# Kernel tuning notes

Measured on AMD Instinct MI355X. Metric: run time of the kernel, lower is better.

The kernel has to match this reference:

```python
import jax, jax.numpy as jnp
import numpy as np

IN_CH = 256
QK_CH = IN_CH // 8  # 32

def setup_inputs() -> dict:
    key = jax.random.key(0)
    ks = jax.random.split(key, 7)
    x = jax.random.normal(ks[0], (4, IN_CH, 64, 64), dtype=jnp.float32)
    s_in = 1.0 / np.sqrt(IN_CH)
    # 1x1 conv weights stored as [out_ch, in_ch]; biases [out_ch]
    Wq = jax.random.uniform(ks[1], (QK_CH, IN_CH), jnp.float32, -s_in, s_in)
    bq = jax.random.uniform(ks[2], (QK_CH,), jnp.float32, -s_in, s_in)
    Wk = jax.random.uniform(ks[3], (QK_CH, IN_CH), jnp.float32, -s_in, s_in)
    bk = jax.random.uniform(ks[4], (QK_CH,), jnp.float32, -s_in, s_in)
    Wv = jax.random.uniform(ks[5], (IN_CH, IN_CH), jnp.float32, -s_in, s_in)
    bv = jax.random.uniform(ks[6], (IN_CH,), jnp.float32, -s_in, s_in)
    return {"x": x, "Wq": Wq, "bq": bq, "Wk": Wk, "bk": bk, "Wv": Wv, "bv": bv}

def reference(x, Wq, bq, Wk, bk, Wv, bv):
    n, c, h, w = x.shape
    xf = x.reshape(n, c, h * w)  # [n, c, hw]
    # 1x1 convs == per-position channel matmuls
    q = jnp.einsum('oc,ncs->nos', Wq, xf) + bq[None, :, None]  # [n, c/8, hw]
    k = jnp.einsum('oc,ncs->nos', Wk, xf) + bk[None, :, None]  # [n, c/8, hw]
    v = jnp.einsum('oc,ncs->nos', Wv, xf) + bv[None, :, None]  # [n, c,  hw]
    # energy[n, i, j] = <q[:, i], k[:, j]>  (no scaling, as in original)
    energy = jnp.einsum('nci,ncj->nij', q, k)  # [n, hw, hw]
    attention = jax.nn.softmax(energy, axis=-1)
    # out[n, c, i] = sum_j v[n, c, j] * attention[n, i, j]
    out = jnp.einsum('ncj,nij->nci', v, attention)
    return out.reshape(n, c, h, w)
```

## Files before the change

### kernel.cpp

```cpp
#include <hip/hip_runtime.h>
#include <hip/hip_bf16.h>
#include <stdint.h>
#include <stddef.h>

typedef unsigned short u16;
typedef unsigned int   u32;
typedef __attribute__((ext_vector_type(8))) short bf16x8;
typedef __attribute__((ext_vector_type(4))) float f32x4;

#define LOG2E   1.44269504f
#define EXP_OFF 23.0831206f

static __device__ __forceinline__ float bf2f(u16 v) {
    u32 u = ((u32)v) << 16; float f; __builtin_memcpy(&f, &u, 4); return f;
}
static __device__ __forceinline__ u16 f2bf(float f) {
    u32 u; __builtin_memcpy(&u, &f, 4);
    u32 r = (u + 0x7fffu + ((u >> 16) & 1u)) >> 16; return (u16)r;
}
static __device__ __forceinline__ float as_f(u32 u) { float f; __builtin_memcpy(&f, &u, 4); return f; }
static __device__ __forceinline__ u32   as_u(float f) { u32 u; __builtin_memcpy(&u, &f, 4); return u; }

static __device__ __forceinline__ int detect_f32_wave0(const void* x, int t) {
    const u32* xw = (const u32*)x;
    int bad = 0;
    #pragma unroll
    for (int k = 0; k < 4; ++k) {
        u32 wv = xw[(t << 2) + k];
        int e = (wv >> 7) & 0xff;
        bad += (e >= 160);
    }
    unsigned long long m = __ballot(bad > 0);
    return (__popcll(m) >= 8) ? 1 : 0;
}


__global__ __launch_bounds__(256) void qkv_proj_mfma(
    const void* __restrict__ x,
    const void* __restrict__ Wq, const void* __restrict__ bq,
    const void* __restrict__ Wk, const void* __restrict__ bk,
    const void* __restrict__ Wv, const void* __restrict__ bv,
    u16* __restrict__ qws, u16* __restrict__ kws, u16* __restrict__ vws,
    int n_off, int nshiftp)
{
    __shared__ u16 Wl[64 * 256];
    __shared__ int dtf;

    const int t    = threadIdx.x;
    const int bid  = blockIdx.x;
    const int n_w  = bid & ((1 << nshiftp) - 1);
    const int rest = bid >> nshiftp;
    const int g    = rest % 5;
    const int it   = rest / 5;
    const int n_g  = n_off + n_w;
    const int i0   = it << 6;

    if (t < 64) { int f = detect_f32_wave0(x, t); if (t == 0) dtf = f; }
    __syncthreads();
    const bool isf32 = (dtf != 0);

    #pragma unroll
    for (int k = 0; k < 16; ++k) {
        int idx  = t + (k << 8);
        int row  = idx >> 6;
        int col4 = (idx & 63) << 2;
        const void* src; int srow;
        if (g == 0) {
            if (row < 32) { src = Wq; srow = row; }
            else          { src = Wk; srow = row - 32; }
        } else { src = Wv; srow = ((g - 1) << 6) + row; }
        ushort4 h;
        if (isf32) {
            float4 wv = *((const float4*)((const float*)src + srow * 256 + col4));
            h.x = f2bf(wv.x); h.y = f2bf(wv.y); h.z = f2bf(wv.z); h.w = f2bf(wv.w);
        } else {
            h = *((const ushort4*)((const u16*)src + srow * 256 + col4));
        }
        *(ushort4*)&Wl[(row << 8) + (col4 ^ ((row & 7) << 3))] = h;
    }
    __syncthreads();

    const int lane = t & 63;
    const int w    = t >> 6;
    const int n16  = lane & 15;
    const int quad = lane >> 4;
    const int i_b  = i0 + (w << 4);
    const int i    = i_b + n16;
    const int swz  = (n16 & 7) << 3;

    f32x4 acc[4];
    #pragma unroll
    for (int f = 0; f < 4; ++f) acc[f] = (f32x4){0.f, 0.f, 0.f, 0.f};

    if (isf32) {
        const float* xp = (const float*)x
            + (((size_t)(n_g * 256 + (quad << 3))) << 12) + i;
        float af[8];
        #pragma unroll
        for (int e = 0; e < 8; ++e) af[e] = xp[(size_t)e << 12];
        #pragma unroll
        for (int c8 = 0; c8 < 8; ++c8) {
            bf16x8 a;
            #pragma unroll
            for (int e = 0; e < 8; ++e) a[e] = (short)f2bf(af[e]);
            if (c8 < 7) {
                const float* xn = xp + (((size_t)(c8 + 1) << 5) << 12);
                #pragma unroll
                for (int e = 0; e < 8; ++e) af[e] = xn[(size_t)e << 12];
            }
            const int c0 = c8 << 5;
            #pragma unroll
            for (int f = 0; f < 4; ++f) {
                const int brow = (f << 4) + n16;
                bf16x8 b = *(const bf16x8*)
                    &Wl[(brow << 8) + ((c0 + (quad << 3)) ^ swz)];
                acc[f] = __builtin_amdgcn_mfma_f32_16x16x32_bf16(a, b, acc[f], 0, 0, 0);
            }
        }
    } else {
        const u16* xp = (const u16*)x
            + (((size_t)(n_g * 256 + (quad << 3))) << 12) + i;
        u16 af[8];
        #pragma unroll
        for (int e = 0; e < 8; ++e) af[e] = xp[(size_t)e << 12];
        #pragma unroll
        for (int c8 = 0; c8 < 8; ++c8) {
            bf16x8 a;
            #pragma unroll
            for (int e = 0; e < 8; ++e) a[e] = (short)af[e];
            if (c8 < 7) {
                const u16* xn = xp + (((size_t)(c8 + 1) << 5) << 12);
                #pragma unroll
                for (int e = 0; e < 8; ++e) af[e] = xn[(size_t)e << 12];
            }
            const int c0 = c8 << 5;
            #pragma unroll
            for (int f = 0; f < 4; ++f) {
                const int brow = (f << 4) + n16;
                bf16x8 b = *(const bf16x8*)
                    &Wl[(brow << 8) + ((c0 + (quad << 3)) ^ swz)];
                acc[f] = __builtin_amdgcn_mfma_f32_16x16x32_bf16(a, b, acc[f], 0, 0, 0);
            }
        }
    }

    if (g == 0) {
        #pragma unroll
        for (int f = 0; f < 4; ++f) {
            const int ol   = (f << 4) + n16;
            const bool isq = (ol < 32);
            const int och  = isq ? ol : (ol - 32);
            float bias;
            if (isf32) bias = ((const float*)(isq ? bq : bk))[och];
            else       bias = bf2f(((const u16*)(isq ? bq : bk))[och]);
            u16* dst = (isq ? qws : kws) + (((size_t)n_w) << 17) + och;
            const float scale = isq ? LOG2E : 1.0f;
            #pragma unroll
            for (int r = 0; r < 4; ++r) {
                const int ii = i_b + (quad << 2) + r;
                dst[(size_t)ii << 5] = f2bf((acc[f][r] + bias) * scale);
            }
        }
    } else {
        #pragma unroll
        for (int f = 0; f < 4; ++f) {
            const int c = ((g - 1) << 6) + (f << 4) + n16;
            float bias = isf32 ? ((const float*)bv)[c]
                               : bf2f(((const u16*)bv)[c]);
            const int i4 = i_b + (quad << 2);
            ushort4 h;
            h.x = f2bf(acc[f][0] + bias);
            h.y = f2bf(acc[f][1] + bias);
            h.z = f2bf(acc[f][2] + bias);
            h.w = f2bf(acc[f][3] + bias);
            const size_t addr = ((size_t)n_w << 20)
                + ((size_t)(c >> 4) << 16)
                + ((size_t)(i4 >> 5) << 9)
                + (size_t)((((((i4 & 31) >> 3) << 4) + (c & 15)) << 3) + (i4 & 7));
            *(ushort4*)(vws + addr) = h;
        }
    }
}

__global__ __launch_bounds__(1024) void flash_mfma6(
    const u16* __restrict__ qws, const u16* __restrict__ kws,
    const u16* __restrict__ vws, void* __restrict__ out,
    const void* __restrict__ x, int n_off, int nshift)
{
    __shared__ __align__(16) char arena[17920];
    __shared__ __align__(16) float lS[64];
    __shared__ int dtf;
    u16*   PsA  = (u16*)arena;
    float* Dbuf = (float*)arena;

    const int t    = threadIdx.x;
    const int lane = t & 63;
    const int w    = t >> 6;
    const int n16  = lane & 15;
    const int quad = lane >> 4;
    const int bid  = blockIdx.x;
    const int n_w  = bid & ((1 << nshift) - 1);
    const int qt   = bid >> nshift;
    const int n_g  = n_off + n_w;
    const int i0   = qt << 6;

    if (t < 64) {
        int f = detect_f32_wave0(x, t);
        if (t == 0) dtf = f;
        lS[t] = 0.f;
    }

    const u16* qb = qws + (((size_t)n_w) << 17);
    const u16* kb = kws + (((size_t)n_w) << 17);
    const u16* vb = vws + (((size_t)n_w) << 20);

    const int qsub_s = w & 3;
    const int jsub   = w >> 2;
    const int cq = w & 7;
    const int jq = w >> 3;

    const bf16x8 qfrag =
        *(const bf16x8*)(qb + ((size_t)(i0 + (qsub_s << 4) + n16) << 5) + (quad << 3));

    f32x4 acc[4][2];
    #pragma unroll
    for (int a = 0; a < 4; ++a)
        #pragma unroll
        for (int b = 0; b < 2; ++b) acc[a][b] = (f32x4){0.f, 0.f, 0.f, 0.f};
    float lp[4] = {0.f, 0.f, 0.f, 0.f};

    const int jcol = (jsub << 4) + n16;
    const int j8   = jcol >> 3;
    const int jlo  = jcol & 7;
    const int ksw  = (jq << 2) + quad;

    const u16* vfp0 = vb + ((size_t)(cq << 1) << 16) + ((size_t)jq << 9)
                         + ((size_t)((quad << 4) + n16) << 3);
    const u16* vfp1 = vfp0 + 65536;

    bf16x8 kreg, vf0, vf1;

    kreg = *(const bf16x8*)(kb + ((size_t)((jsub << 4) + n16) << 5) + (quad << 3));
    {
        u16* Ps = PsA;
        const f32x4 z = {0.f, 0.f, 0.f, 0.f};
        f32x4 s = __builtin_amdgcn_mfma_f32_16x16x32_bf16(qfrag, kreg, z, 0, 0, 0);
        #pragma unroll
        for (int r = 0; r < 4; ++r) {
            const int qrow = (qsub_s << 4) + (quad << 2) + r;
            float p = exp2f(s[r] - EXP_OFF);
            u32 u = as_u(p) & 0xffff0000u;
            lp[r] += as_f(u);
            Ps[qrow * 64 + ((j8 ^ (qrow & 7)) << 3) + jlo] = (u16)(u >> 16);
        }
        kreg = *(const bf16x8*)(kb + ((size_t)(64 + (jsub << 4) + n16) << 5) + (quad << 3));
        vf0 = *(const bf16x8*)(vfp0);
        vf1 = *(const bf16x8*)(vfp1);
    }
    __syncthreads();

    for (int tile = 1; tile < 64; ++tile) {
        const int par  = tile & 1;
        u16* Psc = PsA + (par << 12);
        u16* Psp = PsA + ((par ^ 1) << 12);

        bf16x8 pa[4];
        #pragma unroll
        for (int qs = 0; qs < 4; ++qs) {
            const int qrow = (qs << 4) + n16;
            pa[qs] = *(const bf16x8*)&Psp[qrow * 64 + ((ksw ^ (qrow & 7)) << 3)];
        }
        #pragma unroll
        for (int qs = 0; qs < 4; ++qs) {
            acc[qs][0] = __builtin_amdgcn_mfma_f32_16x16x32_bf16(pa[qs], vf0, acc[qs][0], 0, 0, 0);
            acc[qs][1] = __builtin_amdgcn_mfma_f32_16x16x32_bf16(pa[qs], vf1, acc[qs][1], 0, 0, 0);
        }

        vf0 = *(const bf16x8*)(vfp0 + ((size_t)tile << 10));
        vf1 = *(const bf16x8*)(vfp1 + ((size_t)tile << 10));

        const f32x4 z = {0.f, 0.f, 0.f, 0.f};
        f32x4 s = __builtin_amdgcn_mfma_f32_16x16x32_bf16(qfrag, kreg, z, 0, 0, 0);
        #pragma unroll
        for (int r = 0; r < 4; ++r) {
            const int qrow = (qsub_s << 4) + (quad << 2) + r;
            float p = exp2f(s[r] - EXP_OFF);
            u32 u = as_u(p) & 0xffff0000u;
            lp[r] += as_f(u);
            Psc[qrow * 64 + ((j8 ^ (qrow & 7)) << 3) + jlo] = (u16)(u >> 16);
        }

        if (tile < 63) {
            const int j0n = (tile + 1) << 6;
            kreg = *(const bf16x8*)(kb + ((size_t)(j0n + (jsub << 4) + n16) << 5)
                                    + (quad << 3));
        }
        __syncthreads();
    }

    {
        u16* Psp = PsA + (1 << 12);
        bf16x8 pa[4];
        #pragma unroll
        for (int qs = 0; qs < 4; ++qs) {
            const int qrow = (qs << 4) + n16;
            pa[qs] = *(const bf16x8*)&Psp[qrow * 64 + ((ksw ^ (qrow & 7)) << 3)];
        }
        #pragma unroll
        for (int qs = 0; qs < 4; ++qs) {
            acc[qs][0] = __builtin_amdgcn_mfma_f32_16x16x32_bf16(pa[qs], vf0, acc[qs][0], 0, 0, 0);
            acc[qs][1] = __builtin_amdgcn_mfma_f32_16x16x32_bf16(pa[qs], vf1, acc[qs][1], 0, 0, 0);
        }
    }

    #pragma unroll
    for (int r = 0; r < 4; ++r) {
        lp[r] += __shfl_xor(lp[r], 1);
        lp[r] += __shfl_xor(lp[r], 2);
        lp[r] += __shfl_xor(lp[r], 4);
        lp[r] += __shfl_xor(lp[r], 8);
    }
    if (n16 == 0) {
        #pragma unroll
        for (int r = 0; r < 4; ++r)
            atomicAdd(&lS[(qsub_s << 4) + (quad << 2) + r], lp[r]);
    }
    __syncthreads();
    if (t < 64) lS[t] = 1.0f / lS[t];
    const bool isf32 = (dtf != 0);

    for (int chunk = 0; chunk < 4; ++chunk) {
        __syncthreads();
        if (jq == 1 && (cq >> 1) == chunk) {
            #pragma unroll
            for (int qs = 0; qs < 4; ++qs)
                #pragma unroll
                for (int cs = 0; cs < 2; ++cs)
                    *(f32x4*)&Dbuf[(((cq & 1) << 5) + (cs << 4) + n16) * 68 +
                                   (qs << 4) + (quad << 2)] = acc[qs][cs];
        }
        __syncthreads();
        if (jq == 0 && (cq >> 1) == chunk) {
            #pragma unroll
            for (int qs = 0; qs < 4; ++qs)
                #pragma unroll
                for (int cs = 0; cs < 2; ++cs) {
                    float* p = &Dbuf[(((cq & 1) << 5) + (cs << 4) + n16) * 68 +
                                     (qs << 4) + (quad << 2)];
                    f32x4 d = *(f32x4*)p;
                    d += acc[qs][cs];
                    *(f32x4*)p = d;
                }
        }
        __syncthreads();
        const int c_l = t >> 4;
        const int qg  = (t & 15) << 2;
        float4 d  = *(float4*)&Dbuf[c_l * 68 + qg];
        float4 rl = *(float4*)&lS[qg];
        const int c_glob = (chunk << 6) + c_l;
        const size_t ob = (((size_t)(n_g * 256 + c_glob)) << 12) + i0 + qg;
        if (isf32) {
            float4 o = make_float4(d.x * rl.x, d.y * rl.y, d.z * rl.z, d.w * rl.w);
            *(float4*)((float*)out + ob) = o;
        } else {
            union { uint2 v; u16 h[4]; } o;
            o.h[0] = f2bf(d.x * rl.x);
            o.h[1] = f2bf(d.y * rl.y);
            o.h[2] = f2bf(d.z * rl.z);
            o.h[3] = f2bf(d.w * rl.w);
            *(uint2*)((u16*)out + ob) = o.v;
        }
    }
}

extern "C" void kernel_launch(void* const* d_in, const int* in_sizes, int n_in,
                              void* d_out, int out_size, void* d_ws, size_t ws_size,
                              hipStream_t stream)
{
    const void* x  = d_in[0];
    const void* Wq = d_in[1];
    const void* bq = d_in[2];
    const void* Wk = d_in[3];
    const void* bk = d_in[4];
    const void* Wv = d_in[5];
    const void* bv = d_in[6];

    const size_t full_need = (size_t)(4u * 4096u) * (32 + 32 + 256) * 2;
    if (ws_size >= full_need) {
        u16* qws = (u16*)d_ws;
        u16* kws = qws + (size_t)4 * 4096 * 32;
        u16* vws = kws + (size_t)4 * 4096 * 32;
        qkv_proj_mfma<<<dim3(1280), dim3(256), 0, stream>>>(
            x, Wq, bq, Wk, bk, Wv, bv, qws, kws, vws, 0, 2);
        flash_mfma6<<<dim3(256), dim3(1024), 0, stream>>>(
            qws, kws, vws, d_out, x, 0, 2);
    } else {
        u16* qws = (u16*)d_ws;
        u16* kws = qws + (size_t)4096 * 32;
        u16* vws = kws + (size_t)4096 * 32;
        for (int n = 0; n < 4; ++n) {
            qkv_proj_mfma<<<dim3(320), dim3(256), 0, stream>>>(
                x, Wq, bq, Wk, bk, Wv, bv, qws, kws, vws, n, 0);
            flash_mfma6<<<dim3(64), dim3(1024), 0, stream>>>(
                qws, kws, vws, d_out, x, n, 0);
        }
    }
}
```

Baseline: 144.5 us.

## Halve query tile to 32 rows and drop cross-wave LDS reduction of PV

```diff
diff --git a/kernel.cpp b/kernel.cpp
--- a/kernel.cpp
+++ b/kernel.cpp
@@ -182,16 +182,14 @@
     }
 }
 
-__global__ __launch_bounds__(1024) void flash_mfma6(
+__global__ __launch_bounds__(512) void flash_mfma7(
     const u16* __restrict__ qws, const u16* __restrict__ kws,
     const u16* __restrict__ vws, void* __restrict__ out,
     const void* __restrict__ x, int n_off, int nshift)
 {
-    __shared__ __align__(16) char arena[17920];
-    __shared__ __align__(16) float lS[64];
+    __shared__ __align__(16) u16 PsA[2 * 32 * 64];
+    __shared__ __align__(16) float lS[32];
     __shared__ int dtf;
-    u16*   PsA  = (u16*)arena;
-    float* Dbuf = (float*)arena;
 
     const int t    = threadIdx.x;
     const int lane = t & 63;
@@ -202,29 +200,28 @@
     const int n_w  = bid & ((1 << nshift) - 1);
     const int qt   = bid >> nshift;
     const int n_g  = n_off + n_w;
-    const int i0   = qt << 6;
+    const int i0   = qt << 5;
 
     if (t < 64) {
         int f = detect_f32_wave0(x, t);
         if (t == 0) dtf = f;
-        lS[t] = 0.f;
-    }
+    }
+    if (t < 32) lS[t] = 0.f;
 
     const u16* qb = qws + (((size_t)n_w) << 17);
     const u16* kb = kws + (((size_t)n_w) << 17);
     const u16* vb = vws + (((size_t)n_w) << 20);
 
-    const int qsub_s = w & 3;
-    const int jsub   = w >> 2;
-    const int cq = w & 7;
-    const int jq = w >> 3;
+    const int qsub_s = w & 1;
+    const int jsub   = w >> 1;
+    const int cq = w;
 
     const bf16x8 qfrag =
         *(const bf16x8*)(qb + ((size_t)(i0 + (qsub_s << 4) + n16) << 5) + (quad << 3));
 
-    f32x4 acc[4][2];
-    #pragma unroll
-    for (int a = 0; a < 4; ++a)
+    f32x4 acc[2][2];
+    #pragma unroll
+    for (int a = 0; a < 2; ++a)
         #pragma unroll
         for (int b = 0; b < 2; ++b) acc[a][b] = (f32x4){0.f, 0.f, 0.f, 0.f};
     float lp[4] = {0.f, 0.f, 0.f, 0.f};
@@ -232,59 +229,74 @@
     const int jcol = (jsub << 4) + n16;
     const int j8   = jcol >> 3;
     const int jlo  = jcol & 7;
-    const int ksw  = (jq << 2) + quad;
-
-    const u16* vfp0 = vb + ((size_t)(cq << 1) << 16) + ((size_t)jq << 9)
-                         + ((size_t)((quad << 4) + n16) << 3);
-    const u16* vfp1 = vfp0 + 65536;
-
-    bf16x8 kreg, vf0, vf1;
+
+    const u16* vfp[2][2];
+    #pragma unroll
+    for (int cs = 0; cs < 2; ++cs)
+        #pragma unroll
+        for (int jh = 0; jh < 2; ++jh)
+            vfp[cs][jh] = vb + ((size_t)((cq << 1) + cs) << 16)
+                             + ((size_t)jh << 9)
+                             + ((size_t)((quad << 4) + n16) << 3);
+
+    bf16x8 kreg, vf[2][2];
+    const f32x4 zoff = {-EXP_OFF, -EXP_OFF, -EXP_OFF, -EXP_OFF};
 
     kreg = *(const bf16x8*)(kb + ((size_t)((jsub << 4) + n16) << 5) + (quad << 3));
     {
         u16* Ps = PsA;
-        const f32x4 z = {0.f, 0.f, 0.f, 0.f};
-        f32x4 s = __builtin_amdgcn_mfma_f32_16x16x32_bf16(qfrag, kreg, z, 0, 0, 0);
+        f32x4 s = __builtin_amdgcn_mfma_f32_16x16x32_bf16(qfrag, kreg, zoff, 0, 0, 0);
         #pragma unroll
         for (int r = 0; r < 4; ++r) {
             const int qrow = (qsub_s << 4) + (quad << 2) + r;
-            float p = exp2f(s[r] - EXP_OFF);
+            float p = exp2f(s[r]);
             u32 u = as_u(p) & 0xffff0000u;
             lp[r] += as_f(u);
             Ps[qrow * 64 + ((j8 ^ (qrow & 7)) << 3) + jlo] = (u16)(u >> 16);
         }
         kreg = *(const bf16x8*)(kb + ((size_t)(64 + (jsub << 4) + n16) << 5) + (quad << 3));
-        vf0 = *(const bf16x8*)(vfp0);
-        vf1 = *(const bf16x8*)(vfp1);
+        #pragma unroll
+        for (int cs = 0; cs < 2; ++cs)
+            #pragma unroll
+            for (int jh = 0; jh < 2; ++jh)
+                vf[cs][jh] = *(const bf16x8*)(vfp[cs][jh]);
     }
     __syncthreads();
 
     for (int tile = 1; tile < 64; ++tile) {
         const int par  = tile & 1;
-        u16* Psc = PsA + (par << 12);
-        u16* Psp = PsA + ((par ^ 1) << 12);
-
-        bf16x8 pa[4];
-        #pragma unroll
-        for (int qs = 0; qs < 4; ++qs) {
+        u16* Psc = PsA + (par << 11);
+        u16* Psp = PsA + ((par ^ 1) << 11);
+
+        bf16x8 pa[2][2];
+        #pragma unroll
+        for (int qs = 0; qs < 2; ++qs) {
             const int qrow = (qs << 4) + n16;
-            pa[qs] = *(const bf16x8*)&Psp[qrow * 64 + ((ksw ^ (qrow & 7)) << 3)];
-        }
-        #pragma unroll
-        for (int qs = 0; qs < 4; ++qs) {
-            acc[qs][0] = __builtin_amdgcn_mfma_f32_16x16x32_bf16(pa[qs], vf0, acc[qs][0], 0, 0, 0);
-            acc[qs][1] = __builtin_amdgcn_mfma_f32_16x16x32_bf16(pa[qs], vf1, acc[qs][1], 0, 0, 0);
-        }
-
-        vf0 = *(const bf16x8*)(vfp0 + ((size_t)tile << 10));
-        vf1 = *(const bf16x8*)(vfp1 + ((size_t)tile << 10));
-
-        const f32x4 z = {0.f, 0.f, 0.f, 0.f};
-        f32x4 s = __builtin_amdgcn_mfma_f32_16x16x32_bf16(qfrag, kreg, z, 0, 0, 0);
+            #pragma unroll
+            for (int jh = 0; jh < 2; ++jh) {
+                const int ksw = (jh << 2) + quad;
+                pa[qs][jh] = *(const bf16x8*)&Psp[qrow * 64 + ((ksw ^ (qrow & 7)) << 3)];
+            }
+        }
+        #pragma unroll
+        for (int qs = 0; qs < 2; ++qs)
+            #pragma unroll
+            for (int cs = 0; cs < 2; ++cs) {
+                acc[qs][cs] = __builtin_amdgcn_mfma_f32_16x16x32_bf16(pa[qs][0], vf[cs][0], acc[qs][cs], 0, 0, 0);
+                acc[qs][cs] = __builtin_amdgcn_mfma_f32_16x16x32_bf16(pa[qs][1], vf[cs][1], acc[qs][cs], 0, 0, 0);
+            }
+
+        #pragma unroll
+        for (int cs = 0; cs < 2; ++cs)
+            #pragma unroll
+            for (int jh = 0; jh < 2; ++jh)
+                vf[cs][jh] = *(const bf16x8*)(vfp[cs][jh] + ((size_t)tile << 10));
+
+        f32x4 s = __builtin_amdgcn_mfma_f32_16x16x32_bf16(qfrag, kreg, zoff, 0, 0, 0);
         #pragma unroll
         for (int r = 0; r < 4; ++r) {
             const int qrow = (qsub_s << 4) + (quad << 2) + r;
-            float p = exp2f(s[r] - EXP_OFF);
+            float p = exp2f(s[r]);
             u32 u = as_u(p) & 0xffff0000u;
             lp[r] += as_f(u);
             Psc[qrow * 64 + ((j8 ^ (qrow & 7)) << 3) + jlo] = (u16)(u >> 16);
@@ -299,18 +311,24 @@
     }
 
     {
-        u16* Psp = PsA + (1 << 12);
-        bf16x8 pa[4];
-        #pragma unroll
-        for (int qs = 0; qs < 4; ++qs) {
+        u16* Psp = PsA + (1 << 11);
+        bf16x8 pa[2][2];
+        #pragma unroll
+        for (int qs = 0; qs < 2; ++qs) {
             const int qrow = (qs << 4) + n16;
-            pa[qs] = *(const bf16x8*)&Psp[qrow * 64 + ((ksw ^ (qrow & 7)) << 3)];
-        }
-        #pragma unroll
-        for (int qs = 0; qs < 4; ++qs) {
-            acc[qs][0] = __builtin_amdgcn_mfma_f32_16x16x32_bf16(pa[qs], vf0, acc[qs][0], 0, 0, 0);
-            acc[qs][1] = __builtin_amdgcn_mfma_f32_16x16x32_bf16(pa[qs], vf1, acc[qs][1], 0, 0, 0);
-        }
+            #pragma unroll
+            for (int jh = 0; jh < 2; ++jh) {
+                const int ksw = (jh << 2) + quad;
+                pa[qs][jh] = *(const bf16x8*)&Psp[qrow * 64 + ((ksw ^ (qrow & 7)) << 3)];
+            }
+        }
+        #pragma unroll
+        for (int qs = 0; qs < 2; ++qs)
+            #pragma unroll
+            for (int cs = 0; cs < 2; ++cs) {
+                acc[qs][cs] = __builtin_amdgcn_mfma_f32_16x16x32_bf16(pa[qs][0], vf[cs][0], acc[qs][cs], 0, 0, 0);
+                acc[qs][cs] = __builtin_amdgcn_mfma_f32_16x16x32_bf16(pa[qs][1], vf[cs][1], acc[qs][cs], 0, 0, 0);
+            }
     }
 
     #pragma unroll
@@ -326,49 +344,31 @@
             atomicAdd(&lS[(qsub_s << 4) + (quad << 2) + r], lp[r]);
     }
     __syncthreads();
-    if (t < 64) lS[t] = 1.0f / lS[t];
+    if (t < 32) lS[t] = 1.0f / lS[t];
     const bool isf32 = (dtf != 0);
-
-    for (int chunk = 0; chunk < 4; ++chunk) {
-        __syncthreads();
-        if (jq == 1 && (cq >> 1) == chunk) {
-            #pragma unroll
-            for (int qs = 0; qs < 4; ++qs)
-                #pragma unroll
-                for (int cs = 0; cs < 2; ++cs)
-                    *(f32x4*)&Dbuf[(((cq & 1) << 5) + (cs << 4) + n16) * 68 +
-                                   (qs << 4) + (quad << 2)] = acc[qs][cs];
-        }
-        __syncthreads();
-        if (jq == 0 && (cq >> 1) == chunk) {
-            #pragma unroll
-            for (int qs = 0; qs < 4; ++qs)
-                #pragma unroll
-                for (int cs = 0; cs < 2; ++cs) {
-                    float* p = &Dbuf[(((cq & 1) << 5) + (cs << 4) + n16) * 68 +
-                                     (qs << 4) + (quad << 2)];
-                    f32x4 d = *(f32x4*)p;
-                    d += acc[qs][cs];
-                    *(f32x4*)p = d;
-                }
-        }
-        __syncthreads();
-        const int c_l = t >> 4;
-        const int qg  = (t & 15) << 2;
-        float4 d  = *(float4*)&Dbuf[c_l * 68 + qg];
-        float4 rl = *(float4*)&lS[qg];
-        const int c_glob = (chunk << 6) + c_l;
-        const size_t ob = (((size_t)(n_g * 256 + c_glob)) << 12) + i0 + qg;
-        if (isf32) {
-            float4 o = make_float4(d.x * rl.x, d.y * rl.y, d.z * rl.z, d.w * rl.w);
-            *(float4*)((float*)out + ob) = o;
-        } else {
-            union { uint2 v; u16 h[4]; } o;
-            o.h[0] = f2bf(d.x * rl.x);
-            o.h[1] = f2bf(d.y * rl.y);
-            o.h[2] = f2bf(d.z * rl.z);
-            o.h[3] = f2bf(d.w * rl.w);
-            *(uint2*)((u16*)out + ob) = o.v;
+    __syncthreads();
+
+    #pragma unroll
+    for (int qs = 0; qs < 2; ++qs) {
+        const float4 rl = *(const float4*)&lS[(qs << 4) + (quad << 2)];
+        #pragma unroll
+        for (int cs = 0; cs < 2; ++cs) {
+            const int c = (cq << 5) + (cs << 4) + n16;
+            const int q = i0 + (qs << 4) + (quad << 2);
+            const size_t ob = (((size_t)(n_g * 256 + c)) << 12) + q;
+            const f32x4 d = acc[qs][cs];
+            if (isf32) {
+                float4 o = make_float4(d[0] * rl.x, d[1] * rl.y,
+                                       d[2] * rl.z, d[3] * rl.w);
+                *(float4*)((float*)out + ob) = o;
+            } else {
+                union { uint2 v; u16 h[4]; } o;
+                o.h[0] = f2bf(d[0] * rl.x);
+                o.h[1] = f2bf(d[1] * rl.y);
+                o.h[2] = f2bf(d[2] * rl.z);
+                o.h[3] = f2bf(d[3] * rl.w);
+                *(uint2*)((u16*)out + ob) = o.v;
+            }
         }
     }
 }
@@ -392,7 +392,7 @@
         u16* vws = kws + (size_t)4 * 4096 * 32;
         qkv_proj_mfma<<<dim3(1280), dim3(256), 0, stream>>>(
             x, Wq, bq, Wk, bk, Wv, bv, qws, kws, vws, 0, 2);
-        flash_mfma6<<<dim3(256), dim3(1024), 0, stream>>>(
+        flash_mfma7<<<dim3(512), dim3(512), 0, stream>>>(
             qws, kws, vws, d_out, x, 0, 2);
     } else {
         u16* qws = (u16*)d_ws;
@@ -401,7 +401,7 @@
         for (int n = 0; n < 4; ++n) {
             qkv_proj_mfma<<<dim3(320), dim3(256), 0, stream>>>(
                 x, Wq, bq, Wk, bk, Wv, bv, qws, kws, vws, n, 0);
-            flash_mfma6<<<dim3(64), dim3(1024), 0, stream>>>(
+            flash_mfma7<<<dim3(128), dim3(512), 0, stream>>>(
                 qws, kws, vws, d_out, x, n, 0);
         }
     }
```

Measured after the change: 151.7 us. 1.05x slower.

## Process two key tiles per barrier in flash attention loop

Applied to the files above, without the earlier changes.

```diff
diff --git a/kernel.cpp b/kernel.cpp
--- a/kernel.cpp
+++ b/kernel.cpp
@@ -182,16 +182,48 @@
     }
 }
 
-__global__ __launch_bounds__(1024) void flash_mfma6(
+static __device__ __forceinline__ void s_tile(
+    const bf16x8 qfrag, const bf16x8 kr, u16* __restrict__ Ps,
+    float* __restrict__ lp, int qbase, int j8, int jlo)
+{
+    const f32x4 zoff = {-EXP_OFF, -EXP_OFF, -EXP_OFF, -EXP_OFF};
+    f32x4 s = __builtin_amdgcn_mfma_f32_16x16x32_bf16(qfrag, kr, zoff, 0, 0, 0);
+    #pragma unroll
+    for (int r = 0; r < 4; ++r) {
+        const int qrow = qbase + r;
+        float p = exp2f(s[r]);
+        u32 u = as_u(p) & 0xffff0000u;
+        lp[r] += as_f(u);
+        Ps[qrow * 64 + ((j8 ^ (qrow & 7)) << 3) + jlo] = (u16)(u >> 16);
+    }
+}
+
+static __device__ __forceinline__ void pv_tile(
+    const u16* __restrict__ Ps, const bf16x8 v0, const bf16x8 v1,
+    f32x4 acc[4][2], int n16, int ksw)
+{
+    bf16x8 pa[4];
+    #pragma unroll
+    for (int qs = 0; qs < 4; ++qs) {
+        const int qrow = (qs << 4) + n16;
+        pa[qs] = *(const bf16x8*)&Ps[qrow * 64 + ((ksw ^ (qrow & 7)) << 3)];
+    }
+    #pragma unroll
+    for (int qs = 0; qs < 4; ++qs) {
+        acc[qs][0] = __builtin_amdgcn_mfma_f32_16x16x32_bf16(pa[qs], v0, acc[qs][0], 0, 0, 0);
+        acc[qs][1] = __builtin_amdgcn_mfma_f32_16x16x32_bf16(pa[qs], v1, acc[qs][1], 0, 0, 0);
+    }
+}
+
+__global__ __launch_bounds__(1024) void flash_mfma8(
     const u16* __restrict__ qws, const u16* __restrict__ kws,
     const u16* __restrict__ vws, void* __restrict__ out,
     const void* __restrict__ x, int n_off, int nshift)
 {
-    __shared__ __align__(16) char arena[17920];
+    __shared__ __align__(16) u16 PsA[4 * 64 * 64];
     __shared__ __align__(16) float lS[64];
     __shared__ int dtf;
-    u16*   PsA  = (u16*)arena;
-    float* Dbuf = (float*)arena;
+    float* Dbuf = (float*)PsA;
 
     const int t    = threadIdx.x;
     const int lane = t & 63;
@@ -229,88 +261,59 @@
         for (int b = 0; b < 2; ++b) acc[a][b] = (f32x4){0.f, 0.f, 0.f, 0.f};
     float lp[4] = {0.f, 0.f, 0.f, 0.f};
 
-    const int jcol = (jsub << 4) + n16;
-    const int j8   = jcol >> 3;
-    const int jlo  = jcol & 7;
-    const int ksw  = (jq << 2) + quad;
-
+    const int jcol  = (jsub << 4) + n16;
+    const int j8    = jcol >> 3;
+    const int jlo   = jcol & 7;
+    const int ksw   = (jq << 2) + quad;
+    const int qbase = (qsub_s << 4) + (quad << 2);
+
+    const u16* kp = kb + ((size_t)((jsub << 4) + n16) << 5) + (quad << 3);
     const u16* vfp0 = vb + ((size_t)(cq << 1) << 16) + ((size_t)jq << 9)
                          + ((size_t)((quad << 4) + n16) << 3);
     const u16* vfp1 = vfp0 + 65536;
 
-    bf16x8 kreg, vf0, vf1;
-
-    kreg = *(const bf16x8*)(kb + ((size_t)((jsub << 4) + n16) << 5) + (quad << 3));
+    bf16x8 k0, k1, kn0, kn1, vf00, vf01, vf10, vf11;
+
+    k0 = *(const bf16x8*)(kp);
+    k1 = *(const bf16x8*)(kp + 2048);
+    s_tile(qfrag, k0, PsA,        lp, qbase, j8, jlo);
+    s_tile(qfrag, k1, PsA + 4096, lp, qbase, j8, jlo);
+    kn0 = *(const bf16x8*)(kp + 2 * 2048);
+    kn1 = *(const bf16x8*)(kp + 3 * 2048);
+    __syncthreads();
+
+    for (int p = 1; p < 32; ++p) {
+        k0 = kn0; k1 = kn1;
+        if (p < 31) {
+            kn0 = *(const bf16x8*)(kp + ((size_t)((p << 1) + 2) << 11));
+            kn1 = *(const bf16x8*)(kp + ((size_t)((p << 1) + 3) << 11));
+        }
+        const size_t tA = (size_t)((p << 1) - 2) << 10;
+        const size_t tB = (size_t)((p << 1) - 1) << 10;
+        vf00 = *(const bf16x8*)(vfp0 + tA);
+        vf01 = *(const bf16x8*)(vfp1 + tA);
+        vf10 = *(const bf16x8*)(vfp0 + tB);
+        vf11 = *(const bf16x8*)(vfp1 + tB);
+
+        u16* PsW0 = PsA + ((p & 1) << 13);
+        u16* PsW1 = PsW0 + 4096;
+        u16* PsR0 = PsA + (((p & 1) << 13) ^ 8192);
+        u16* PsR1 = PsR0 + 4096;
+
+        s_tile(qfrag, k0, PsW0, lp, qbase, j8, jlo);
+        s_tile(qfrag, k1, PsW1, lp, qbase, j8, jlo);
+        pv_tile(PsR0, vf00, vf01, acc, n16, ksw);
+        pv_tile(PsR1, vf10, vf11, acc, n16, ksw);
+        __syncthreads();
+    }
+
     {
-        u16* Ps = PsA;
-        const f32x4 z = {0.f, 0.f, 0.f, 0.f};
-        f32x4 s = __builtin_amdgcn_mfma_f32_16x16x32_bf16(qfrag, kreg, z, 0, 0, 0);
-        #pragma unroll
-        for (int r = 0; r < 4; ++r) {
-            const int qrow = (qsub_s << 4) + (quad << 2) + r;
-            float p = exp2f(s[r] - EXP_OFF);
-            u32 u = as_u(p) & 0xffff0000u;
-            lp[r] += as_f(u);
-            Ps[qrow * 64 + ((j8 ^ (qrow & 7)) << 3) + jlo] = (u16)(u >> 16);
-        }
-        kreg = *(const bf16x8*)(kb + ((size_t)(64 + (jsub << 4) + n16) << 5) + (quad << 3));
-        vf0 = *(const bf16x8*)(vfp0);
-        vf1 = *(const bf16x8*)(vfp1);
-    }
-    __syncthreads();
-
-    for (int tile = 1; tile < 64; ++tile) {
-        const int par  = tile & 1;
-        u16* Psc = PsA + (par << 12);
-        u16* Psp = PsA + ((par ^ 1) << 12);
-
-        bf16x8 pa[4];
-        #pragma unroll
-        for (int qs = 0; qs < 4; ++qs) {
-            const int qrow = (qs << 4) + n16;
-            pa[qs] = *(const bf16x8*)&Psp[qrow * 64 + ((ksw ^ (qrow & 7)) << 3)];
-        }
-        #pragma unroll
-        for (int qs = 0; qs < 4; ++qs) {
-            acc[qs][0] = __builtin_amdgcn_mfma_f32_16x16x32_bf16(pa[qs], vf0, acc[qs][0], 0, 0, 0);
-            acc[qs][1] = __builtin_amdgcn_mfma_f32_16x16x32_bf16(pa[qs], vf1, acc[qs][1], 0, 0, 0);
-        }
-
-        vf0 = *(const bf16x8*)(vfp0 + ((size_t)tile << 10));
-        vf1 = *(const bf16x8*)(vfp1 + ((size_t)tile << 10));
-
-        const f32x4 z = {0.f, 0.f, 0.f, 0.f};
-        f32x4 s = __builtin_amdgcn_mfma_f32_16x16x32_bf16(qfrag, kreg, z, 0, 0, 0);
-        #pragma unroll
-        for (int r = 0; r < 4; ++r) {
-            const int qrow = (qsub_s << 4) + (quad << 2) + r;
-            float p = exp2f(s[r] - EXP_OFF);
-            u32 u = as_u(p) & 0xffff0000u;
-            lp[r] += as_f(u);
-            Psc[qrow * 64 + ((j8 ^ (qrow & 7)) << 3) + jlo] = (u16)(u >> 16);
-        }
-
-        if (tile < 63) {
-            const int j0n = (tile + 1) << 6;
-            kreg = *(const bf16x8*)(kb + ((size_t)(j0n + (jsub << 4) + n16) << 5)
-                                    + (quad << 3));
-        }
-        __syncthreads();
-    }
-
-    {
-        u16* Psp = PsA + (1 << 12);
-        bf16x8 pa[4];
-        #pragma unroll
-        for (int qs = 0; qs < 4; ++qs) {
-            const int qrow = (qs << 4) + n16;
-            pa[qs] = *(const bf16x8*)&Psp[qrow * 64 + ((ksw ^ (qrow & 7)) << 3)];
-        }
-        #pragma unroll
-        for (int qs = 0; qs < 4; ++qs) {
-            acc[qs][0] = __builtin_amdgcn_mfma_f32_16x16x32_bf16(pa[qs], vf0, acc[qs][0], 0, 0, 0);
-            acc[qs][1] = __builtin_amdgcn_mfma_f32_16x16x32_bf16(pa[qs], vf1, acc[qs][1], 0, 0, 0);
-        }
+        vf00 = *(const bf16x8*)(vfp0 + ((size_t)62 << 10));
+        vf01 = *(const bf16x8*)(vfp1 + ((size_t)62 << 10));
+        vf10 = *(const bf16x8*)(vfp0 + ((size_t)63 << 10));
+        vf11 = *(const bf16x8*)(vfp1 + ((size_t)63 << 10));
+        pv_tile(PsA + 2 * 4096, vf00, vf01, acc, n16, ksw);
+        pv_tile(PsA + 3 * 4096, vf10, vf11, acc, n16, ksw);
     }
 
     #pragma unroll
@@ -323,7 +326,7 @@
     if (n16 == 0) {
         #pragma unroll
         for (int r = 0; r < 4; ++r)
-            atomicAdd(&lS[(qsub_s << 4) + (quad << 2) + r], lp[r]);
+            atomicAdd(&lS[qbase + r], lp[r]);
     }
     __syncthreads();
     if (t < 64) lS[t] = 1.0f / lS[t];
@@ -392,7 +395,7 @@
         u16* vws = kws + (size_t)4 * 4096 * 32;
         qkv_proj_mfma<<<dim3(1280), dim3(256), 0, stream>>>(
             x, Wq, bq, Wk, bk, Wv, bv, qws, kws, vws, 0, 2);
-        flash_mfma6<<<dim3(256), dim3(1024), 0, stream>>>(
+        flash_mfma8<<<dim3(256), dim3(1024), 0, stream>>>(
             qws, kws, vws, d_out, x, 0, 2);
     } else {
         u16* qws = (u16*)d_ws;
@@ -401,7 +404,7 @@
         for (int n = 0; n < 4; ++n) {
             qkv_proj_mfma<<<dim3(320), dim3(256), 0, stream>>>(
                 x, Wq, bq, Wk, bk, Wv, bv, qws, kws, vws, n, 0);
-            flash_mfma6<<<dim3(64), dim3(1024), 0, stream>>>(
+            flash_mfma8<<<dim3(64), dim3(1024), 0, stream>>>(
                 qws, kws, vws, d_out, x, n, 0);
         }
     }
```

New measurement: 150.7 us. 1.04x slower.
